# Kernel tuning notes

Hardware: AMD Instinct MI355X
Metric: run time of the kernel (lower is better)

## Reference

```python
import jax, jax.numpy as jnp
import numpy as np

BLOCK = 64      # sparse block size (power of 2, >= 16)
NB = 128        # number of blocks -> max_seqlen = 8192
LOCAL = 8       # causal local window, in blocks
GLOBAL = 1      # leading global blocks every query attends to
K = LOCAL + GLOBAL
SM_SCALE = 1.0 / np.sqrt(64.0)  # default sm_scale = 1/sqrt(head_dim)


def _build_layout():
    # Fixed-width equivalent of the CSR block layout: for query block i,
    # live key blocks are the GLOBAL leading blocks plus the LOCAL-wide
    # causal window ending at i. Entries outside [0, i] are masked invalid;
    # global entries that fall inside the local window are invalidated to
    # avoid double counting.
    rows = np.arange(NB)[:, None]
    loc = rows - np.arange(LOCAL - 1, -1, -1)[None, :]      # [NB, LOCAL], ascending, ends at i
    glb = np.tile(np.arange(GLOBAL)[None, :], (NB, 1))      # [NB, GLOBAL]
    loc_valid = loc >= 0
    glb_valid = glb < (rows - LOCAL + 1)                    # strictly below local window
    col = np.concatenate([glb, np.maximum(loc, 0)], axis=1)  # [NB, K]
    valid = np.concatenate([glb_valid, loc_valid], axis=1)   # [NB, K]
    return col.astype(np.int32), valid


def setup_inputs() -> dict:
    key = jax.random.key(0)
    kq, kk, kv = jax.random.split(key, 3)
    B, S, H, D = 2, NB * BLOCK, 16, 64
    q = jax.random.normal(kq, (B, S, H, D), jnp.float32)
    k = jax.random.normal(kk, (B, S, H, D), jnp.float32)
    v = jax.random.normal(kv, (B, S, H, D), jnp.float32)
    col, valid = _build_layout()
    return {"q": q, "k": k, "v": v,
            "col_idx": jnp.asarray(col), "col_valid": jnp.asarray(valid)}


def reference(q, k, v, col_idx, col_valid):
    # Block-sparse causal attention. Only key/value blocks listed in
    # col_idx (where col_valid) are touched; token-level causal mask is
    # applied inside the gathered blocks (diagonal blocks get intra-block
    # causal masking, matching the kernel's behavior).
    B, S, H, D = q.shape
    bs = BLOCK
    nb = S // bs
    qb = q.reshape(B, nb, bs, H, D)                       # [B, nb, bs, H, D]
    kb = k.reshape(B, nb, bs, H, D)[:, col_idx]           # [B, nb, K, bs, H, D]
    vb = v.reshape(B, nb, bs, H, D)[:, col_idx]
    scores = jnp.einsum('bimhd,bijnhd->bhimjn', qb, kb) * SM_SCALE  # [B,H,nb,bs,K,bs]
    qpos = jnp.arange(nb)[:, None] * bs + jnp.arange(bs)[None, :]          # [nb, bs]
    kpos = col_idx[:, :, None] * bs + jnp.arange(bs)[None, None, :]        # [nb, K, bs]
    mask = (kpos[:, None, :, :] <= qpos[:, :, None, None]) & col_valid[:, None, :, None]
    neg = jnp.finfo(scores.dtype).min
    scores = jnp.where(mask[None, None], scores, neg)
    shp = scores.shape
    p = jax.nn.softmax(scores.reshape(shp[0], shp[1], shp[2], shp[3], -1), axis=-1).reshape(shp)
    out = jnp.einsum('bhimjn,bijnhd->bimhd', p, vb)       # [B, nb, bs, H, D]
    return out.reshape(B, S, H, D)
```

## Files before the change

### kernel.cpp

```cpp
#include <hip/hip_runtime.h>
#include <hip/hip_bf16.h>

#define NBQ     128
#define NLOCAL  8
#define NH      16
#define NBATCH  2
#define DIM     64
#define SEQ     (NBQ * 64)
#define PPAD    72
#define QK_SCALE 0.1803368801111204f

typedef __attribute__((ext_vector_type(8))) short bf16x8;
typedef __attribute__((ext_vector_type(4))) float f32x4;
typedef __attribute__((ext_vector_type(2))) unsigned int u32x2;

__device__ inline short f2b(float x) {
    unsigned int u = __float_as_uint(x);
    return (short)((u + 0x8000u) >> 16);
}
__device__ inline unsigned int pack2(unsigned int lo_rnd, unsigned int hi_rnd) {
    return __builtin_amdgcn_perm(hi_rnd, lo_rnd, 0x07060302u);
}

__global__ __launch_bounds__(256) void sparse_attn_kernel(
    const float* __restrict__ Q, const float* __restrict__ Kg,
    const float* __restrict__ Vg, float* __restrict__ Out)
{
    __shared__ __align__(16) short sK [64 * 64];
    __shared__ __align__(16) short sVt[64 * 64];
    __shared__ __align__(16) short sP [4 * 16 * PPAD];

    const int qb  = blockIdx.x >> 5;
    const int bh  = blockIdx.x & 31;
    const int b   = bh >> 4;
    const int h   = bh & 15;
    const int tid  = threadIdx.x;
    const int wave = tid >> 6;
    const int lane = tid & 63;
    const int quad = lane >> 4;
    const int l15  = lane & 15;

    const int sg   = tid >> 4;
    const int t15c = tid & 15;
    const int tok4 = sg << 2;
    const int ft4  = t15c << 2;

    bf16x8 qf[2];
    {
        const int qrow = qb * 64 + wave * 16 + l15;
        const float* qp = Q + (((size_t)(b * SEQ + qrow)) * NH + h) * DIM;
#pragma unroll
        for (int ks = 0; ks < 2; ++ks) {
            const float* p = qp + ks * 32 + quad * 8;
            const f32x4 x0 = *(const f32x4*)(p);
            const f32x4 x1 = *(const f32x4*)(p + 4);
            bf16x8 f;
#pragma unroll
            for (int c = 0; c < 4; ++c) {
                f[c]     = f2b(x0[c] * QK_SCALE);
                f[c + 4] = f2b(x1[c] * QK_SCALE);
            }
            qf[ks] = f;
        }
    }

    float l_part[4];
    f32x4 o_acc[4];
#pragma unroll
    for (int r = 0; r < 4; ++r) l_part[r] = 0.f;
#pragma unroll
    for (int ft = 0; ft < 4; ++ft) o_acc[ft] = (f32x4){0.f, 0.f, 0.f, 0.f};

    const int gsw = l15 & 14;

    for (int j = 0; j < 9; ++j) {
        int kb; bool valid;
        if (j == 0) { kb = 0; valid = (qb >= NLOCAL); }
        else        { kb = qb - 8 + j; valid = (kb >= 0); }
        if (!valid) continue;
        const bool diag = (kb == qb);

        {
            const size_t basekv = (((size_t)(b * SEQ + kb * 64 + tok4)) * NH + h) * DIM + ft4;
            unsigned int kr[4][4], vr[4][4];
#pragma unroll
            for (int i = 0; i < 4; ++i) {
                const f32x4 kx = *(const f32x4*)(Kg + basekv + (size_t)i * (NH * DIM));
                const f32x4 vx = *(const f32x4*)(Vg + basekv + (size_t)i * (NH * DIM));
#pragma unroll
                for (int c = 0; c < 4; ++c) {
                    kr[i][c] = __float_as_uint(kx[c]) + 0x8000u;
                    vr[i][c] = __float_as_uint(vx[c]) + 0x8000u;
                }
            }
#pragma unroll
            for (int i = 0; i < 4; ++i) {
                const int row = tok4 + i;
                const int cp  = t15c ^ (row & 14);
                u32x2 w;
                w.x = pack2(kr[i][0], kr[i][1]);
                w.y = pack2(kr[i][2], kr[i][3]);
                *(u32x2*)&sK[row * 64 + cp * 4] = w;
            }
#pragma unroll
            for (int c = 0; c < 4; ++c) {
                const int row = ft4 + c;
                const int cp  = sg ^ (row & 14);
                u32x2 w;
                w.x = pack2(vr[0][c], vr[1][c]);
                w.y = pack2(vr[2][c], vr[3][c]);
                *(u32x2*)&sVt[row * 64 + cp * 4] = w;
            }
        }
        __syncthreads();

        f32x4 s[4];
#pragma unroll
        for (int nt = 0; nt < 4; ++nt) {
            const int row = (nt * 16 + l15) * 64;
            const bf16x8 k0 = *(const bf16x8*)&sK[row + (((quad * 2)     ^ gsw) << 2)];
            const bf16x8 k1 = *(const bf16x8*)&sK[row + (((8 + quad * 2) ^ gsw) << 2)];
            f32x4 acc = (f32x4){0.f, 0.f, 0.f, 0.f};
            acc = __builtin_amdgcn_mfma_f32_16x16x32_bf16(qf[0], k0, acc, 0, 0, 0);
            acc = __builtin_amdgcn_mfma_f32_16x16x32_bf16(qf[1], k1, acc, 0, 0, 0);
            s[nt] = acc;
        }

        bf16x8 vf[8];
#pragma unroll
        for (int ft = 0; ft < 4; ++ft) {
            const int row = (ft * 16 + l15) * 64;
            vf[2 * ft]     = *(const bf16x8*)&sVt[row + (((quad * 2)     ^ gsw) << 2)];
            vf[2 * ft + 1] = *(const bf16x8*)&sVt[row + (((8 + quad * 2) ^ gsw) << 2)];
        }

        if (diag) {
#pragma unroll
            for (int nt = 0; nt < 4; ++nt) {
                const int ki = nt * 16 + l15;
#pragma unroll
                for (int r = 0; r < 4; ++r) {
                    const int qi = wave * 16 + quad * 4 + r;
                    if (ki > qi) s[nt][r] = -1e30f;
                }
            }
        }

#pragma unroll
        for (int r = 0; r < 4; ++r) {
            float ps = 0.f;
#pragma unroll
            for (int nt = 0; nt < 4; ++nt) {
                const float p = exp2f(s[nt][r]);
                s[nt][r] = p;
                ps += p;
            }
            l_part[r] += ps;
        }

        short* pbase = &sP[wave * 16 * PPAD];
#pragma unroll
        for (int nt = 0; nt < 4; ++nt)
#pragma unroll
            for (int r = 0; r < 4; ++r)
                pbase[(quad * 4 + r) * PPAD + nt * 16 + l15] = f2b(s[nt][r]);
        __syncthreads();
        const bf16x8 pf0 = *(const bf16x8*)&pbase[l15 * PPAD + quad * 8];
        const bf16x8 pf1 = *(const bf16x8*)&pbase[l15 * PPAD + 32 + quad * 8];

#pragma unroll
        for (int ft = 0; ft < 4; ++ft) {
            o_acc[ft] = __builtin_amdgcn_mfma_f32_16x16x32_bf16(pf0, vf[2 * ft],     o_acc[ft], 0, 0, 0);
            o_acc[ft] = __builtin_amdgcn_mfma_f32_16x16x32_bf16(pf1, vf[2 * ft + 1], o_acc[ft], 0, 0, 0);
        }
    }

#pragma unroll
    for (int r = 0; r < 4; ++r) {
        float l = l_part[r];
        l += __shfl_xor(l, 1);
        l += __shfl_xor(l, 2);
        l += __shfl_xor(l, 4);
        l += __shfl_xor(l, 8);
        const float inv = 1.0f / l;
        const int qrow = qb * 64 + wave * 16 + quad * 4 + r;
        float* op = Out + (((size_t)(b * SEQ + qrow)) * NH + h) * DIM;
#pragma unroll
        for (int ft = 0; ft < 4; ++ft)
            op[ft * 16 + l15] = o_acc[ft][r] * inv;
    }
}

extern "C" void kernel_launch(void* const* d_in, const int* in_sizes, int n_in,
                              void* d_out, int out_size, void* d_ws, size_t ws_size,
                              hipStream_t stream) {
    const float* q = (const float*)d_in[0];
    const float* k = (const float*)d_in[1];
    const float* v = (const float*)d_in[2];
    float* out = (float*)d_out;
    dim3 grid(NBQ * NBATCH * NH);
    sparse_attn_kernel<<<grid, dim3(256), 0, stream>>>(q, k, v, out);
}
```

Before: 261.1 us.

## Compute transposed S^T so P stays in registers; double-buffer K/V LDS

Swaps the MFMA operand order so each lane holds a column of S^T, which lets the exp'd probabilities be packed straight into bf16 register fragments for 16x16x16 MFMAs against V. This removes the shared-memory round trip for P and the second __syncthreads per key block. K/V shared buffers are double-buffered by iteration parity, and the loop iterates only over valid blocks. Output stores become 16-byte vector writes, and launch bounds request 4 blocks per CU, which may constrain registers.

Measured after the change: 261.0 us. About the same (-0.1%).

```diff
diff --git a/kernel.cpp b/kernel.cpp
--- a/kernel.cpp
+++ b/kernel.cpp
@@ -7,10 +7,10 @@
 #define NBATCH  2
 #define DIM     64
 #define SEQ     (NBQ * 64)
-#define PPAD    72
 #define QK_SCALE 0.1803368801111204f
 
 typedef __attribute__((ext_vector_type(8))) short bf16x8;
+typedef __attribute__((ext_vector_type(4))) short short4v;
 typedef __attribute__((ext_vector_type(4))) float f32x4;
 typedef __attribute__((ext_vector_type(2))) unsigned int u32x2;
 
@@ -22,13 +22,14 @@
     return __builtin_amdgcn_perm(hi_rnd, lo_rnd, 0x07060302u);
 }
 
-__global__ __launch_bounds__(256) void sparse_attn_kernel(
+typedef union { u32x2 u; short4v s; } pk_u;
+
+__global__ __launch_bounds__(256, 4) void sparse_attn_kernel(
     const float* __restrict__ Q, const float* __restrict__ Kg,
     const float* __restrict__ Vg, float* __restrict__ Out)
 {
-    __shared__ __align__(16) short sK [64 * 64];
-    __shared__ __align__(16) short sVt[64 * 64];
-    __shared__ __align__(16) short sP [4 * 16 * PPAD];
+    __shared__ __align__(16) short sK [2][64 * 64];
+    __shared__ __align__(16) short sVt[2][64 * 64];
 
     const int qb  = blockIdx.x >> 5;
     const int bh  = blockIdx.x & 31;
@@ -64,29 +65,32 @@
         }
     }
 
-    float l_part[4];
+    float l_part = 0.f;
     f32x4 o_acc[4];
-#pragma unroll
-    for (int r = 0; r < 4; ++r) l_part[r] = 0.f;
 #pragma unroll
     for (int ft = 0; ft < 4; ++ft) o_acc[ft] = (f32x4){0.f, 0.f, 0.f, 0.f};
 
     const int gsw = l15 & 14;
+    const float* kbase = Kg + (size_t)b * (SEQ * NH * DIM);
+    const float* vbase = Vg + (size_t)b * (SEQ * NH * DIM);
+    const unsigned off0 = (unsigned)((tok4 * NH + h) * DIM + ft4);
 
-    for (int j = 0; j < 9; ++j) {
-        int kb; bool valid;
-        if (j == 0) { kb = 0; valid = (qb >= NLOCAL); }
-        else        { kb = qb - 8 + j; valid = (kb >= 0); }
-        if (!valid) continue;
-        const bool diag = (kb == qb);
+    const int kb_lo = (qb - 7 > 0) ? (qb - 7) : 0;
+    const int has_g = (qb >= NLOCAL) ? 1 : 0;
+    const int niter = (qb - kb_lo + 1) + has_g;
+
+    for (int it = 0; it < niter; ++it) {
+        const int kb = (it < has_g) ? 0 : (kb_lo + it - has_g);
+        short* sKb = &sK [it & 1][0];
+        short* sVb = &sVt[it & 1][0];
 
         {
-            const size_t basekv = (((size_t)(b * SEQ + kb * 64 + tok4)) * NH + h) * DIM + ft4;
+            const unsigned koff = ((unsigned)kb << 16) + off0;
             unsigned int kr[4][4], vr[4][4];
 #pragma unroll
             for (int i = 0; i < 4; ++i) {
-                const f32x4 kx = *(const f32x4*)(Kg + basekv + (size_t)i * (NH * DIM));
-                const f32x4 vx = *(const f32x4*)(Vg + basekv + (size_t)i * (NH * DIM));
+                const f32x4 kx = *(const f32x4*)(kbase + koff + i * (NH * DIM));
+                const f32x4 vx = *(const f32x4*)(vbase + koff + i * (NH * DIM));
 #pragma unroll
                 for (int c = 0; c < 4; ++c) {
                     kr[i][c] = __float_as_uint(kx[c]) + 0x8000u;
@@ -100,7 +104,7 @@
                 u32x2 w;
                 w.x = pack2(kr[i][0], kr[i][1]);
                 w.y = pack2(kr[i][2], kr[i][3]);
-                *(u32x2*)&sK[row * 64 + cp * 4] = w;
+                *(u32x2*)&sKb[row * 64 + cp * 4] = w;
             }
 #pragma unroll
             for (int c = 0; c < 4; ++c) {
@@ -109,7 +113,7 @@
                 u32x2 w;
                 w.x = pack2(vr[0][c], vr[1][c]);
                 w.y = pack2(vr[2][c], vr[3][c]);
-                *(u32x2*)&sVt[row * 64 + cp * 4] = w;
+                *(u32x2*)&sVb[row * 64 + cp * 4] = w;
             }
         }
         __syncthreads();
@@ -118,77 +122,64 @@
 #pragma unroll
         for (int nt = 0; nt < 4; ++nt) {
             const int row = (nt * 16 + l15) * 64;
-            const bf16x8 k0 = *(const bf16x8*)&sK[row + (((quad * 2)     ^ gsw) << 2)];
-            const bf16x8 k1 = *(const bf16x8*)&sK[row + (((8 + quad * 2) ^ gsw) << 2)];
+            const bf16x8 k0 = *(const bf16x8*)&sKb[row + (((2 * quad)     ^ gsw) << 2)];
+            const bf16x8 k1 = *(const bf16x8*)&sKb[row + (((8 + 2 * quad) ^ gsw) << 2)];
             f32x4 acc = (f32x4){0.f, 0.f, 0.f, 0.f};
-            acc = __builtin_amdgcn_mfma_f32_16x16x32_bf16(qf[0], k0, acc, 0, 0, 0);
-            acc = __builtin_amdgcn_mfma_f32_16x16x32_bf16(qf[1], k1, acc, 0, 0, 0);
+            acc = __builtin_amdgcn_mfma_f32_16x16x32_bf16(k0, qf[0], acc, 0, 0, 0);
+            acc = __builtin_amdgcn_mfma_f32_16x16x32_bf16(k1, qf[1], acc, 0, 0, 0);
             s[nt] = acc;
         }
 
-        bf16x8 vf[8];
+        if (kb == qb) {
+            const int qi = wave * 16 + l15;
+#pragma unroll
+            for (int nt = 0; nt < 4; ++nt)
+#pragma unroll
+                for (int r = 0; r < 4; ++r) {
+                    const int ki = nt * 16 + quad * 4 + r;
+                    if (ki > qi) s[nt][r] = -1e30f;
+                }
+        }
+
+        short4v pb[4];
+#pragma unroll
+        for (int nt = 0; nt < 4; ++nt) {
+            float ps = 0.f;
+            unsigned int pr[4];
+#pragma unroll
+            for (int r = 0; r < 4; ++r) {
+                const float p = exp2f(s[nt][r]);
+                ps += p;
+                pr[r] = __float_as_uint(p) + 0x8000u;
+            }
+            l_part += ps;
+            pk_u pw;
+            pw.u.x = pack2(pr[0], pr[1]);
+            pw.u.y = pack2(pr[2], pr[3]);
+            pb[nt] = pw.s;
+        }
+
 #pragma unroll
         for (int ft = 0; ft < 4; ++ft) {
             const int row = (ft * 16 + l15) * 64;
-            vf[2 * ft]     = *(const bf16x8*)&sVt[row + (((quad * 2)     ^ gsw) << 2)];
-            vf[2 * ft + 1] = *(const bf16x8*)&sVt[row + (((8 + quad * 2) ^ gsw) << 2)];
-        }
-
-        if (diag) {
+            f32x4 acc = o_acc[ft];
 #pragma unroll
             for (int nt = 0; nt < 4; ++nt) {
-                const int ki = nt * 16 + l15;
-#pragma unroll
-                for (int r = 0; r < 4; ++r) {
-                    const int qi = wave * 16 + quad * 4 + r;
-                    if (ki > qi) s[nt][r] = -1e30f;
-                }
+                const short4v va = *(const short4v*)&sVb[row + (((4 * nt + quad) ^ gsw) << 2)];
+                acc = __builtin_amdgcn_mfma_f32_16x16x16bf16_1k(va, pb[nt], acc, 0, 0, 0);
             }
-        }
-
-#pragma unroll
-        for (int r = 0; r < 4; ++r) {
-            float ps = 0.f;
-#pragma unroll
-            for (int nt = 0; nt < 4; ++nt) {
-                const float p = exp2f(s[nt][r]);
-                s[nt][r] = p;
-                ps += p;
-            }
-            l_part[r] += ps;
-        }
-
-        short* pbase = &sP[wave * 16 * PPAD];
-#pragma unroll
-        for (int nt = 0; nt < 4; ++nt)
-#pragma unroll
-            for (int r = 0; r < 4; ++r)
-                pbase[(quad * 4 + r) * PPAD + nt * 16 + l15] = f2b(s[nt][r]);
-        __syncthreads();
-        const bf16x8 pf0 = *(const bf16x8*)&pbase[l15 * PPAD + quad * 8];
-        const bf16x8 pf1 = *(const bf16x8*)&pbase[l15 * PPAD + 32 + quad * 8];
-
-#pragma unroll
-        for (int ft = 0; ft < 4; ++ft) {
-            o_acc[ft] = __builtin_amdgcn_mfma_f32_16x16x32_bf16(pf0, vf[2 * ft],     o_acc[ft], 0, 0, 0);
-            o_acc[ft] = __builtin_amdgcn_mfma_f32_16x16x32_bf16(pf1, vf[2 * ft + 1], o_acc[ft], 0, 0, 0);
+            o_acc[ft] = acc;
         }
     }
 
+    l_part += __shfl_xor(l_part, 16);
+    l_part += __shfl_xor(l_part, 32);
+    const float inv = 1.0f / l_part;
+    const int qrow = qb * 64 + wave * 16 + l15;
+    float* op = Out + (((size_t)(b * SEQ + qrow)) * NH + h) * DIM + quad * 4;
 #pragma unroll
-    for (int r = 0; r < 4; ++r) {
-        float l = l_part[r];
-        l += __shfl_xor(l, 1);
-        l += __shfl_xor(l, 2);
-        l += __shfl_xor(l, 4);
-        l += __shfl_xor(l, 8);
-        const float inv = 1.0f / l;
-        const int qrow = qb * 64 + wave * 16 + quad * 4 + r;
-        float* op = Out + (((size_t)(b * SEQ + qrow)) * NH + h) * DIM;
-#pragma unroll
-        for (int ft = 0; ft < 4; ++ft)
-            op[ft * 16 + l15] = o_acc[ft][r] * inv;
-    }
+    for (int ft = 0; ft < 4; ++ft)
+        *(f32x4*)(op + ft * 16) = o_acc[ft] * inv;
 }
 
 extern "C" void kernel_launch(void* const* d_in, const int* in_sizes, int n_in,
```
